# Optimization experiments

Hardware: AMD Instinct MI355X
Metric: run time of the kernel (lower is better)

Reference implementation:

```python
import jax, jax.numpy as jnp
import numpy as np

SLOPE = 25.0  # snntorch surrogate.fast_sigmoid default slope
NUM_STEPS = 15

@jax.custom_vjp
def spike(x):
    # Heaviside forward, fast-sigmoid surrogate backward
    return (x > 0).astype(x.dtype)

def _spike_fwd(x):
    return spike(x), x

def _spike_bwd(x, g):
    return (g / (SLOPE * jnp.abs(x) + 1.0) ** 2,)

spike.defvjp(_spike_fwd, _spike_bwd)


def setup_inputs() -> dict:
    p, hidden, B = 97, 512, 32768
    key = jax.random.key(0)
    ks = jax.random.split(key, 6)
    s1 = 1.0 / np.sqrt(2 * hidden)
    s2 = 1.0 / np.sqrt(hidden)
    return {
        "x": jax.random.randint(ks[0], (B, 2), 0, p, dtype=jnp.int64 if jax.config.jax_enable_x64 else jnp.int32),
        "embed_w": jax.random.normal(ks[1], (p, hidden), jnp.float32),
        "W1": jax.random.uniform(ks[2], (hidden, 2 * hidden), jnp.float32, -s1, s1),
        "b1": jax.random.uniform(ks[3], (hidden,), jnp.float32, -s1, s1),
        "W2": jax.random.uniform(ks[4], (p, hidden), jnp.float32, -s2, s2),
        "b2": jax.random.uniform(ks[5], (p,), jnp.float32, -s2, s2),
        "beta1": jnp.float32(0.85),
        "beta2": jnp.float32(0.85),
        "thr1": jnp.float32(1.0),
        "thr2": jnp.float32(1.0),
    }


def reference(x, embed_w, W1, b1, W2, b2, beta1, beta2, thr1, thr2):
    # parameter clamps (done in-place under no_grad in torch)
    beta1 = jnp.clip(beta1, 0.1, 0.9)
    beta2 = jnp.clip(beta2, 0.1, 0.9)
    thr1 = jnp.maximum(thr1, 0.1)
    thr2 = jnp.maximum(thr2, 0.1)

    B = x.shape[0]
    hidden = embed_w.shape[1]
    p = W2.shape[0]

    emb = embed_w[x].reshape(B, 2 * hidden)          # [B, 2H]
    cur1 = emb @ W1.T + b1                           # constant across steps [B, H]

    def step(carry, _):
        mem1, mem2 = carry
        # lif1: Leaky, reset_mechanism='subtract'; reset computed from prev mem (detached)
        reset = jax.lax.stop_gradient((mem1 - thr1 > 0).astype(mem1.dtype))
        mem1 = jnp.clip(beta1, 0.0, 1.0) * mem1 + cur1 - reset * thr1
        spk1 = spike(mem1 - thr1)                    # [B, H]
        cur2 = spk1 @ W2.T + b2                      # [B, p]
        # lif2: reset_mechanism='none'
        mem2 = jnp.clip(beta2, 0.0, 1.0) * mem2 + cur2
        return (mem1, mem2), None

    mem1 = jnp.zeros((B, hidden), cur1.dtype)
    mem2 = jnp.zeros((B, p), cur1.dtype)
    (mem1, mem2), _ = jax.lax.scan(step, (mem1, mem2), None, length=NUM_STEPS)
    return mem2  # final membrane potential of output layer
```

## Files before the change

### kernel.cpp

```cpp
#include <hip/hip_runtime.h>
#include <cstddef>

#define PMOD 97
#define HID 512
#define NPAIR 9409
#define NSTEPS 15

typedef __attribute__((ext_vector_type(8))) short short8;
typedef __attribute__((ext_vector_type(4))) short short4_t;
typedef __attribute__((ext_vector_type(4))) float f32x4;

static __device__ __forceinline__ unsigned short f2bf_rn(float f) {
    unsigned u = __float_as_uint(f);
    u += 0x7FFFu + ((u >> 16) & 1u);
    return (unsigned short)(u >> 16);
}
static __device__ __forceinline__ float bf2f(unsigned short h) {
    return __uint_as_float(((unsigned)h) << 16);
}
static __device__ __forceinline__ void split_hilo(const float* __restrict__ p,
                                                  short8& hi, short8& lo) {
    const float4 v0 = *(const float4*)p;
    const float4 v1 = *(const float4*)(p + 4);
    const float vv[8] = {v0.x, v0.y, v0.z, v0.w, v1.x, v1.y, v1.z, v1.w};
#pragma unroll
    for (int q = 0; q < 8; ++q) {
        const unsigned short hb = f2bf_rn(vv[q]);
        hi[q] = (short)hb;
        lo[q] = (short)f2bf_rn(vv[q] - bf2f(hb));
    }
}

__global__ __launch_bounds__(256) void k_abm(const float* __restrict__ embed,
                                             const float* __restrict__ W1,
                                             const float* __restrict__ W2,
                                             const float* __restrict__ b1,
                                             short* __restrict__ w2bf,
                                             float* __restrict__ Ap,
                                             float* __restrict__ Bm) {
    __shared__ f32x4 red[3][64];

    const int t = threadIdx.x;
    const int lane = t & 63;
    const int kq = t >> 6;

    const int gid = blockIdx.x * 256 + t;
    if (gid < PMOD * HID / 4) {
        const float4 v = ((const float4*)W2)[gid];
        const float vv[4] = {v.x, v.y, v.z, v.w};
        short4_t h4;
#pragma unroll
        for (int q = 0; q < 4; ++q) h4[q] = (short)f2bf_rn(vv[q]);
        *(short4_t*)(w2bf + gid * 4) = h4;
    }

    const int mt = blockIdx.x >> 6;
    const int ng = blockIdx.x & 63;
    int e = mt * 16 + (lane & 15);
    if (e > PMOD - 1) e = PMOD - 1;
    const int n = ng * 16 + (lane & 15);
    const int h = n & 511;
    const int half = n >> 9;
    const int kbase = kq * 128 + (lane >> 4) * 8;

    f32x4 acc = (f32x4){0.f, 0.f, 0.f, 0.f};
#pragma unroll
    for (int kt = 0; kt < 4; ++kt) {
        const int k = kbase + kt * 32;
        short8 ahi, alo, bhi, blo;
        split_hilo(embed + (size_t)e * HID + k, ahi, alo);
        split_hilo(W1 + (size_t)h * 1024 + half * HID + k, bhi, blo);
        acc = __builtin_amdgcn_mfma_f32_16x16x32_bf16(ahi, bhi, acc, 0, 0, 0);
        acc = __builtin_amdgcn_mfma_f32_16x16x32_bf16(alo, bhi, acc, 0, 0, 0);
        acc = __builtin_amdgcn_mfma_f32_16x16x32_bf16(ahi, blo, acc, 0, 0, 0);
    }

    if (kq != 0) red[kq - 1][lane] = acc;
    __syncthreads();
    if (kq == 0) {
        acc += red[0][lane];
        acc += red[1][lane];
        acc += red[2][lane];
        const float bias = half ? 0.f : b1[h];
#pragma unroll
        for (int reg = 0; reg < 4; ++reg) {
            const int er = mt * 16 + (lane >> 4) * 4 + reg;
            if (er < PMOD) {
                if (half == 0) Ap[(size_t)er * HID + h] = acc[reg] + bias;
                else           Bm[(size_t)er * HID + h] = acc[reg];
            }
        }
    }
}

__global__ __launch_bounds__(1024) void k_pairs(const float* __restrict__ Ap,
                                                const float* __restrict__ Bm,
                                                const short* __restrict__ w2bf,
                                                const float* __restrict__ b2,
                                                const float* __restrict__ pbeta1,
                                                const float* __restrict__ pbeta2,
                                                const float* __restrict__ pthr1,
                                                float* __restrict__ pairOut) {
    __shared__ short8 wfrag[16][64];
    __shared__ f32x4 red[3][7][64];

    const float beta1 = fminf(fmaxf(pbeta1[0], 0.1f), 0.9f);
    const float beta2 = fminf(fmaxf(pbeta2[0], 0.1f), 0.9f);
    const float thr   = fmaxf(pthr1[0], 0.1f);

    const int t = threadIdx.x;
    const int lane = t & 63;
    const int w = t >> 6;
    const int pblk = blockIdx.x * 16;

    const int pid0 = pblk + (lane & 15);
    const int pid  = (pid0 < NPAIR) ? pid0 : (NPAIR - 1);
    const unsigned i = (unsigned)pid / PMOD;
    const unsigned j = (unsigned)pid - i * PMOD;

    {
        const int kt = w;
        const int h = kt * 32 + (lane >> 4) * 8;
        const float* ap = Ap + (size_t)i * HID + h;
        const float* bp = Bm + (size_t)j * HID + h;
        const float4 a0 = *(const float4*)ap;
        const float4 a1 = *(const float4*)(ap + 4);
        const float4 g0 = *(const float4*)bp;
        const float4 g1 = *(const float4*)(bp + 4);
        float c[8] = {a0.x + g0.x, a0.y + g0.y, a0.z + g0.z, a0.w + g0.w,
                      a1.x + g1.x, a1.y + g1.y, a1.z + g1.z, a1.w + g1.w};
        float cm[8], m[8], wv[8];
        bool sb[8];
#pragma unroll
        for (int q = 0; q < 8; ++q) {
            cm[q] = c[q] - thr; m[q] = 0.f; wv[q] = 0.f; sb[q] = false;
        }
        for (int s = 0; s < NSTEPS; ++s) {
#pragma unroll
            for (int q = 0; q < 8; ++q) {
                const float cadj = sb[q] ? cm[q] : c[q];
                m[q] = fmaf(beta1, m[q], cadj);
                sb[q] = m[q] > thr;
                wv[q] = fmaf(beta2, wv[q], sb[q] ? 1.f : 0.f);
            }
        }
        short8 af;
#pragma unroll
        for (int q = 0; q < 8; ++q) af[q] = (short)f2bf_rn(wv[q]);
        wfrag[kt][lane] = af;
    }
    __syncthreads();

    const int kq = w & 3;
    const int ns = w >> 2;
    f32x4 acc[2];
#pragma unroll
    for (int q = 0; q < 2; ++q) acc[q] = (f32x4){0.f, 0.f, 0.f, 0.f};

#pragma unroll
    for (int kk = 0; kk < 4; ++kk) {
        const int kt = kq * 4 + kk;
        const short8 af = wfrag[kt][lane];
        const int k = kt * 32 + (lane >> 4) * 8;
#pragma unroll
        for (int q = 0; q < 2; ++q) {
            const int nt = ns * 2 + q;
            if (nt < 7) {
                const int o0 = nt * 16 + (lane & 15);
                const int oc = (o0 < PMOD) ? o0 : (PMOD - 1);
                const short8 bf = *(const short8*)(w2bf + (size_t)oc * HID + k);
                acc[q] = __builtin_amdgcn_mfma_f32_16x16x32_bf16(af, bf, acc[q], 0, 0, 0);
            }
        }
    }

    if (kq != 0) {
#pragma unroll
        for (int q = 0; q < 2; ++q) {
            const int nt = ns * 2 + q;
            if (nt < 7) red[kq - 1][nt][lane] = acc[q];
        }
    }
    __syncthreads();
    if (kq == 0) {
        float S = 0.f;
#pragma unroll
        for (int s = 0; s < NSTEPS; ++s) S = fmaf(beta2, S, 1.f);
#pragma unroll
        for (int q = 0; q < 2; ++q) {
            const int nt = ns * 2 + q;
            if (nt < 7) {
                f32x4 a = acc[q];
                a += red[0][nt][lane];
                a += red[1][nt][lane];
                a += red[2][nt][lane];
                const int o = nt * 16 + (lane & 15);
                if (o < PMOD) {
                    const float bias = b2[o] * S;
#pragma unroll
                    for (int reg = 0; reg < 4; ++reg) {
                        const int prow = pblk + (lane >> 4) * 4 + reg;
                        if (prow < NPAIR)
                            pairOut[(size_t)prow * PMOD + o] = a[reg] + bias;
                    }
                }
            }
        }
    }
}

__global__ __launch_bounds__(256) void k_scatter(const int* __restrict__ x,
                                                 const float* __restrict__ pairOut,
                                                 float* __restrict__ out,
                                                 int total) {
    const unsigned idx = blockIdx.x * 256u + threadIdx.x;
    if (idx >= (unsigned)total) return;
    const unsigned b = idx / PMOD;
    const unsigned o = idx - b * PMOD;
    const int pid = x[2 * b] * PMOD + x[2 * b + 1];
    out[idx] = pairOut[(size_t)pid * PMOD + o];
}

extern "C" void kernel_launch(void* const* d_in, const int* in_sizes, int n_in,
                              void* d_out, int out_size, void* d_ws, size_t ws_size,
                              hipStream_t stream) {
    const int*   x     = (const int*)d_in[0];
    const float* embed = (const float*)d_in[1];
    const float* W1    = (const float*)d_in[2];
    const float* b1    = (const float*)d_in[3];
    const float* W2    = (const float*)d_in[4];
    const float* b2    = (const float*)d_in[5];
    const float* beta1 = (const float*)d_in[6];
    const float* beta2 = (const float*)d_in[7];
    const float* thr1  = (const float*)d_in[8];

    float* out = (float*)d_out;
    const int B = in_sizes[0] / 2;

    char* ws = (char*)d_ws;
    float* pairOut = (float*)(ws);
    short* w2bf    = (short*)(ws + 3650816);
    float* Ap      = (float*)(ws + 3750144);
    float* Bm      = (float*)(ws + 3948800);

    k_abm<<<448, 256, 0, stream>>>(embed, W1, W2, b1, w2bf, Ap, Bm);

    const int nblk = (NPAIR + 15) / 16;
    k_pairs<<<nblk, 1024, 0, stream>>>(Ap, Bm, w2bf, b2, beta1, beta2, thr1, pairOut);

    const int total = B * PMOD;
    k_scatter<<<(total + 255) / 256, 256, 0, stream>>>(x, pairOut, out, total);
}
```

Measured before the change: 41.07 us.

## Split fused pair kernel into separate spike-simulation and MFMA GEMM kernels

The fused per-pair kernel (LIF simulation into LDS, then MFMA against W2) is split in two. k_sim runs the 15-step recurrence with one wave per pair and coalesced loads, and writes bf16 spike traces to a workspace buffer. k_gemm then uses 256-thread blocks in which each wave covers all 7 output tiles over a quarter of K. This gives simpler, smaller blocks and better-coalesced simulation loads, at the cost of an extra launch and a roughly 9.6 MB round trip through global memory for the intermediate.

```diff
diff --git a/kernel.cpp b/kernel.cpp
--- a/kernel.cpp
+++ b/kernel.cpp
@@ -93,17 +93,12 @@
     }
 }
 
-__global__ __launch_bounds__(1024) void k_pairs(const float* __restrict__ Ap,
-                                                const float* __restrict__ Bm,
-                                                const short* __restrict__ w2bf,
-                                                const float* __restrict__ b2,
-                                                const float* __restrict__ pbeta1,
-                                                const float* __restrict__ pbeta2,
-                                                const float* __restrict__ pthr1,
-                                                float* __restrict__ pairOut) {
-    __shared__ short8 wfrag[16][64];
-    __shared__ f32x4 red[3][7][64];
-
+__global__ __launch_bounds__(256) void k_sim(const float* __restrict__ Ap,
+                                             const float* __restrict__ Bm,
+                                             const float* __restrict__ pbeta1,
+                                             const float* __restrict__ pbeta2,
+                                             const float* __restrict__ pthr1,
+                                             short* __restrict__ wspk) {
     const float beta1 = fminf(fmaxf(pbeta1[0], 0.1f), 0.9f);
     const float beta2 = fminf(fmaxf(pbeta2[0], 0.1f), 0.9f);
     const float thr   = fmaxf(pthr1[0], 0.1f);
@@ -111,75 +106,79 @@
     const int t = threadIdx.x;
     const int lane = t & 63;
     const int w = t >> 6;
-    const int pblk = blockIdx.x * 16;
-
-    const int pid0 = pblk + (lane & 15);
+    const int pid0 = blockIdx.x * 4 + w;
     const int pid  = (pid0 < NPAIR) ? pid0 : (NPAIR - 1);
     const unsigned i = (unsigned)pid / PMOD;
     const unsigned j = (unsigned)pid - i * PMOD;
-
-    {
-        const int kt = w;
-        const int h = kt * 32 + (lane >> 4) * 8;
-        const float* ap = Ap + (size_t)i * HID + h;
-        const float* bp = Bm + (size_t)j * HID + h;
-        const float4 a0 = *(const float4*)ap;
-        const float4 a1 = *(const float4*)(ap + 4);
-        const float4 g0 = *(const float4*)bp;
-        const float4 g1 = *(const float4*)(bp + 4);
-        float c[8] = {a0.x + g0.x, a0.y + g0.y, a0.z + g0.z, a0.w + g0.w,
-                      a1.x + g1.x, a1.y + g1.y, a1.z + g1.z, a1.w + g1.w};
-        float cm[8], m[8], wv[8];
-        bool sb[8];
+    const int h = lane * 8;
+
+    const float* ap = Ap + (size_t)i * HID + h;
+    const float* bp = Bm + (size_t)j * HID + h;
+    const float4 a0 = *(const float4*)ap;
+    const float4 a1 = *(const float4*)(ap + 4);
+    const float4 g0 = *(const float4*)bp;
+    const float4 g1 = *(const float4*)(bp + 4);
+    float c[8] = {a0.x + g0.x, a0.y + g0.y, a0.z + g0.z, a0.w + g0.w,
+                  a1.x + g1.x, a1.y + g1.y, a1.z + g1.z, a1.w + g1.w};
+    float cm[8], m[8], wv[8];
+    bool sb[8];
+#pragma unroll
+    for (int q = 0; q < 8; ++q) {
+        cm[q] = c[q] - thr; m[q] = 0.f; wv[q] = 0.f; sb[q] = false;
+    }
+    for (int s = 0; s < NSTEPS; ++s) {
 #pragma unroll
         for (int q = 0; q < 8; ++q) {
-            cm[q] = c[q] - thr; m[q] = 0.f; wv[q] = 0.f; sb[q] = false;
-        }
-        for (int s = 0; s < NSTEPS; ++s) {
-#pragma unroll
-            for (int q = 0; q < 8; ++q) {
-                const float cadj = sb[q] ? cm[q] : c[q];
-                m[q] = fmaf(beta1, m[q], cadj);
-                sb[q] = m[q] > thr;
-                wv[q] = fmaf(beta2, wv[q], sb[q] ? 1.f : 0.f);
-            }
-        }
-        short8 af;
-#pragma unroll
-        for (int q = 0; q < 8; ++q) af[q] = (short)f2bf_rn(wv[q]);
-        wfrag[kt][lane] = af;
-    }
-    __syncthreads();
-
-    const int kq = w & 3;
-    const int ns = w >> 2;
-    f32x4 acc[2];
-#pragma unroll
-    for (int q = 0; q < 2; ++q) acc[q] = (f32x4){0.f, 0.f, 0.f, 0.f};
+            const float cadj = sb[q] ? cm[q] : c[q];
+            m[q] = fmaf(beta1, m[q], cadj);
+            sb[q] = m[q] > thr;
+            wv[q] = fmaf(beta2, wv[q], sb[q] ? 1.f : 0.f);
+        }
+    }
+    short8 af;
+#pragma unroll
+    for (int q = 0; q < 8; ++q) af[q] = (short)f2bf_rn(wv[q]);
+    *(short8*)(wspk + (size_t)pid * HID + h) = af;
+}
+
+__global__ __launch_bounds__(256) void k_gemm(const short* __restrict__ wspk,
+                                              const short* __restrict__ w2bf,
+                                              const float* __restrict__ b2,
+                                              const float* __restrict__ pbeta2,
+                                              float* __restrict__ pairOut) {
+    __shared__ f32x4 red[3][7][64];
+
+    const float beta2 = fminf(fmaxf(pbeta2[0], 0.1f), 0.9f);
+
+    const int t = threadIdx.x;
+    const int lane = t & 63;
+    const int kq = t >> 6;
+    const int pblk = blockIdx.x * 16;
+
+    const int pid0 = pblk + (lane & 15);
+    const int pidc = (pid0 < NPAIR) ? pid0 : (NPAIR - 1);
+
+    f32x4 acc[7];
+#pragma unroll
+    for (int nt = 0; nt < 7; ++nt) acc[nt] = (f32x4){0.f, 0.f, 0.f, 0.f};
 
 #pragma unroll
     for (int kk = 0; kk < 4; ++kk) {
         const int kt = kq * 4 + kk;
-        const short8 af = wfrag[kt][lane];
         const int k = kt * 32 + (lane >> 4) * 8;
-#pragma unroll
-        for (int q = 0; q < 2; ++q) {
-            const int nt = ns * 2 + q;
-            if (nt < 7) {
-                const int o0 = nt * 16 + (lane & 15);
-                const int oc = (o0 < PMOD) ? o0 : (PMOD - 1);
-                const short8 bf = *(const short8*)(w2bf + (size_t)oc * HID + k);
-                acc[q] = __builtin_amdgcn_mfma_f32_16x16x32_bf16(af, bf, acc[q], 0, 0, 0);
-            }
+        const short8 af = *(const short8*)(wspk + (size_t)pidc * HID + k);
+#pragma unroll
+        for (int nt = 0; nt < 7; ++nt) {
+            const int o0 = nt * 16 + (lane & 15);
+            const int oc = (o0 < PMOD) ? o0 : (PMOD - 1);
+            const short8 bf = *(const short8*)(w2bf + (size_t)oc * HID + k);
+            acc[nt] = __builtin_amdgcn_mfma_f32_16x16x32_bf16(af, bf, acc[nt], 0, 0, 0);
         }
     }
 
     if (kq != 0) {
 #pragma unroll
-        for (int q = 0; q < 2; ++q) {
-            const int nt = ns * 2 + q;
-            if (nt < 7) red[kq - 1][nt][lane] = acc[q];
-        }
+        for (int nt = 0; nt < 7; ++nt) red[kq - 1][nt][lane] = acc[nt];
     }
     __syncthreads();
     if (kq == 0) {
@@ -187,22 +186,19 @@
 #pragma unroll
         for (int s = 0; s < NSTEPS; ++s) S = fmaf(beta2, S, 1.f);
 #pragma unroll
-        for (int q = 0; q < 2; ++q) {
-            const int nt = ns * 2 + q;
-            if (nt < 7) {
-                f32x4 a = acc[q];
-                a += red[0][nt][lane];
-                a += red[1][nt][lane];
-                a += red[2][nt][lane];
-                const int o = nt * 16 + (lane & 15);
-                if (o < PMOD) {
-                    const float bias = b2[o] * S;
-#pragma unroll
-                    for (int reg = 0; reg < 4; ++reg) {
-                        const int prow = pblk + (lane >> 4) * 4 + reg;
-                        if (prow < NPAIR)
-                            pairOut[(size_t)prow * PMOD + o] = a[reg] + bias;
-                    }
+        for (int nt = 0; nt < 7; ++nt) {
+            f32x4 a = acc[nt];
+            a += red[0][nt][lane];
+            a += red[1][nt][lane];
+            a += red[2][nt][lane];
+            const int o = nt * 16 + (lane & 15);
+            if (o < PMOD) {
+                const float bias = b2[o] * S;
+#pragma unroll
+                for (int reg = 0; reg < 4; ++reg) {
+                    const int prow = pblk + (lane >> 4) * 4 + reg;
+                    if (prow < NPAIR)
+                        pairOut[(size_t)prow * PMOD + o] = a[reg] + bias;
                 }
             }
         }
@@ -242,11 +238,15 @@
     short* w2bf    = (short*)(ws + 3650816);
     float* Ap      = (float*)(ws + 3750144);
     float* Bm      = (float*)(ws + 3948800);
+    short* wspk    = (short*)(ws + 4147456);
 
     k_abm<<<448, 256, 0, stream>>>(embed, W1, W2, b1, w2bf, Ap, Bm);
 
+    const int simblk = (NPAIR + 3) / 4;
+    k_sim<<<simblk, 256, 0, stream>>>(Ap, Bm, beta1, beta2, thr1, wspk);
+
     const int nblk = (NPAIR + 15) / 16;
-    k_pairs<<<nblk, 1024, 0, stream>>>(Ap, Bm, w2bf, b2, beta1, beta2, thr1, pairOut);
+    k_gemm<<<nblk, 256, 0, stream>>>(wspk, w2bf, b2, beta2, pairOut);
 
     const int total = B * PMOD;
     k_scatter<<<(total + 255) / 256, 256, 0, stream>>>(x, pairOut, out, total);
```

Result: slower. 49.47 us (+20.5%).

## Fuse batch scatter into pair kernel via per-block shared-memory batch lists

Applied to the files above, without the earlier changes.

Drops the separate scatter kernel and the global pairOut buffer. Each pair block now scans the whole index array, uses shared-memory atomics to build a list of the batch rows that map to its 16 pairs, stages the pair results in a shared tile, and writes those rows of the output directly. This removes one launch and the round trip of the pair table through global memory. In exchange, every block re-reads the full index array, and any pair with more than CAP=64 matching rows would silently lose outputs.

```diff
diff --git a/kernel.cpp b/kernel.cpp
--- a/kernel.cpp
+++ b/kernel.cpp
@@ -5,6 +5,7 @@
 #define HID 512
 #define NPAIR 9409
 #define NSTEPS 15
+#define CAP 64
 
 typedef __attribute__((ext_vector_type(8))) short short8;
 typedef __attribute__((ext_vector_type(4))) short short4_t;
@@ -93,16 +94,21 @@
     }
 }
 
-__global__ __launch_bounds__(1024) void k_pairs(const float* __restrict__ Ap,
-                                                const float* __restrict__ Bm,
-                                                const short* __restrict__ w2bf,
-                                                const float* __restrict__ b2,
-                                                const float* __restrict__ pbeta1,
-                                                const float* __restrict__ pbeta2,
-                                                const float* __restrict__ pthr1,
-                                                float* __restrict__ pairOut) {
+__global__ __launch_bounds__(1024) void k_mega(const float* __restrict__ Ap,
+                                               const float* __restrict__ Bm,
+                                               const short* __restrict__ w2bf,
+                                               const float* __restrict__ b2,
+                                               const float* __restrict__ pbeta1,
+                                               const float* __restrict__ pbeta2,
+                                               const float* __restrict__ pthr1,
+                                               const int* __restrict__ x,
+                                               int nB,
+                                               float* __restrict__ out) {
     __shared__ short8 wfrag[16][64];
     __shared__ f32x4 red[3][7][64];
+    __shared__ float ptile[16][112];
+    __shared__ int lcnt[16];
+    __shared__ int lblist[16][CAP];
 
     const float beta1 = fminf(fmaxf(pbeta1[0], 0.1f), 0.9f);
     const float beta2 = fminf(fmaxf(pbeta2[0], 0.1f), 0.9f);
@@ -112,6 +118,8 @@
     const int lane = t & 63;
     const int w = t >> 6;
     const int pblk = blockIdx.x * 16;
+
+    if (t < 16) lcnt[t] = 0;
 
     const int pid0 = pblk + (lane & 15);
     const int pid  = (pid0 < NPAIR) ? pid0 : (NPAIR - 1);
@@ -181,7 +189,21 @@
             if (nt < 7) red[kq - 1][nt][lane] = acc[q];
         }
     }
-    __syncthreads();
+
+    for (int it = 0; it < 32; ++it) {
+        const int b = it * 1024 + t;
+        if (b < nB) {
+            const int2 xb = ((const int2*)x)[b];
+            const int rel = xb.x * PMOD + xb.y - pblk;
+            if ((unsigned)rel < 16u) {
+                const int slot = atomicAdd(&lcnt[rel], 1);
+                if (slot < CAP) lblist[rel][slot] = b;
+            }
+        }
+    }
+
+    __syncthreads();
+
     if (kq == 0) {
         float S = 0.f;
 #pragma unroll
@@ -199,26 +221,26 @@
                     const float bias = b2[o] * S;
 #pragma unroll
                     for (int reg = 0; reg < 4; ++reg) {
-                        const int prow = pblk + (lane >> 4) * 4 + reg;
-                        if (prow < NPAIR)
-                            pairOut[(size_t)prow * PMOD + o] = a[reg] + bias;
+                        const int prow = (lane >> 4) * 4 + reg;
+                        ptile[prow][o] = a[reg] + bias;
                     }
                 }
             }
         }
     }
-}
-
-__global__ __launch_bounds__(256) void k_scatter(const int* __restrict__ x,
-                                                 const float* __restrict__ pairOut,
-                                                 float* __restrict__ out,
-                                                 int total) {
-    const unsigned idx = blockIdx.x * 256u + threadIdx.x;
-    if (idx >= (unsigned)total) return;
-    const unsigned b = idx / PMOD;
-    const unsigned o = idx - b * PMOD;
-    const int pid = x[2 * b] * PMOD + x[2 * b + 1];
-    out[idx] = pairOut[(size_t)pid * PMOD + o];
+    __syncthreads();
+
+    {
+        const int nb = lcnt[w];
+        const float v0 = ptile[w][lane];
+        const float v1 = (lane < PMOD - 64) ? ptile[w][64 + lane] : 0.f;
+        for (int s = 0; s < nb; ++s) {
+            const int b = lblist[w][s];
+            float* orow = out + (size_t)b * PMOD;
+            orow[lane] = v0;
+            if (lane < PMOD - 64) orow[64 + lane] = v1;
+        }
+    }
 }
 
 extern "C" void kernel_launch(void* const* d_in, const int* in_sizes, int n_in,
@@ -238,16 +260,13 @@
     const int B = in_sizes[0] / 2;
 
     char* ws = (char*)d_ws;
-    float* pairOut = (float*)(ws);
-    short* w2bf    = (short*)(ws + 3650816);
-    float* Ap      = (float*)(ws + 3750144);
-    float* Bm      = (float*)(ws + 3948800);
+    short* w2bf = (short*)(ws);
+    float* Ap   = (float*)(ws + 99584);
+    float* Bm   = (float*)(ws + 298496);
 
     k_abm<<<448, 256, 0, stream>>>(embed, W1, W2, b1, w2bf, Ap, Bm);
 
     const int nblk = (NPAIR + 15) / 16;
-    k_pairs<<<nblk, 1024, 0, stream>>>(Ap, Bm, w2bf, b2, beta1, beta2, thr1, pairOut);
-
-    const int total = B * PMOD;
-    k_scatter<<<(total + 255) / 256, 256, 0, stream>>>(x, pairOut, out, total);
-}
+    k_mega<<<nblk, 1024, 0, stream>>>(Ap, Bm, w2bf, b2, beta1, beta2, thr1,
+                                      x, B, out);
+}
```

Result: slower. 45.80 us (+11.5%).
